# Optimization experiments

Hardware: AMD Instinct MI355X
Metric: run time of the kernel (lower is better)

## Reference

```python
import jax, jax.numpy as jnp
import numpy as np

FS = 512.0
T = 2048
CYC_PHA, CYC_AMP = 3, 6
NBINS = 18
PHA_BANDS = [(2.0 + 2.0 * k, 4.0 + 2.0 * k) for k in range(10)]
AMP_BANDS = [(30.0 + 12.0 * k, 42.0 + 12.0 * k) for k in range(10)]


def _design_filter(fs, low, high, cycle):
    # windowed-sinc bandpass, taps = cycle * fs / low (tensorpac cycle rule), forced odd
    n = int(cycle * fs / low)
    if n % 2 == 0:
        n += 1
    t = np.arange(n) - (n - 1) / 2.0
    lp = lambda fc: 2.0 * fc / fs * np.sinc(2.0 * fc / fs * t)
    h = (lp(high) - lp(low)) * np.hamming(n)
    fc = 0.5 * (low + high)
    h = h / np.abs(np.sum(h * np.exp(-2j * np.pi * fc / fs * t)))  # unit gain at band center
    return h.astype(np.float32)


def _build_kernels():
    filts = [_design_filter(FS, l, h, CYC_PHA) for l, h in PHA_BANDS] + \
            [_design_filter(FS, l, h, CYC_AMP) for l, h in AMP_BANDS]
    L = max(f.shape[0] for f in filts)
    padded = []
    for f in filts:
        p = L - f.shape[0]
        pl = p // 2
        padded.append(np.pad(f, (pl, p - pl)))
    return np.stack(padded)  # (F, L), L odd


def _conv_same(sig, kernels):
    # sig: (N, Tp), kernels: (F, L) -> (N, F, Tp); cross-correlation, 'same' padding (L odd)
    L = kernels.shape[1]
    pad = (L - 1) // 2
    return jax.lax.conv_general_dilated(
        sig[:, None, :], kernels[:, None, :], window_strides=(1,),
        padding=((pad, L - 1 - pad),), dimension_numbers=("NCH", "OIH", "NCH"))


def _analytic(x):
    # FFT-based Hilbert analytic signal along last axis
    n = x.shape[-1]
    h = np.zeros(n, np.float32)
    h[0] = 1.0
    if n % 2 == 0:
        h[n // 2] = 1.0
        h[1:n // 2] = 2.0
    else:
        h[1:(n + 1) // 2] = 2.0
    return jnp.fft.ifft(jnp.fft.fft(x, axis=-1) * h, axis=-1)


def _modulation_index(pha, amp):
    # Tort MI: pha (B,C,P,S,T), amp (B,C,A,S,T) -> (B,C,P,A)
    idx = jnp.clip(jnp.floor((pha + jnp.pi) / (2.0 * jnp.pi) * NBINS), 0, NBINS - 1).astype(jnp.int32)
    sums, cnts = [], []
    for b in range(NBINS):  # fixed small bin count
        m = (idx == b).astype(amp.dtype)                       # (B,C,P,S,T)
        sums.append(jnp.einsum('bcpst,bcast->bcpas', m, amp))  # (B,C,P,A,S)
        cnts.append(m.sum(-1))                                 # (B,C,P,S)
    amp_sum = jnp.stack(sums, -1)                              # (B,C,P,A,S,N)
    cnt = jnp.stack(cnts, -1)[:, :, :, None, :, :]             # (B,C,P,1,S,N)
    amp_mean = amp_sum / jnp.maximum(cnt, 1.0)
    p = amp_mean / jnp.maximum(amp_mean.sum(-1, keepdims=True), 1e-12)
    log_n = jnp.log(jnp.asarray(NBINS, amp.dtype))
    mi = (log_n + (p * jnp.log(jnp.maximum(p, 1e-12))).sum(-1)) / log_n
    return mi.mean(-1)  # average over segments


def setup_inputs() -> dict:
    key = jax.random.key(0)
    x = jax.random.normal(key, (4, 8, 4, T), dtype=jnp.float32)
    kernels = jnp.asarray(_build_kernels())
    return {"x": x, "kernels": kernels}


def reference(x, kernels):
    B, C, S, Tlen = x.shape
    npha = len(PHA_BANDS)
    pad = kernels.shape[1] - 1  # max_padlen (edge_mode)
    sig = x.reshape(B * C * S, Tlen)
    sig = jnp.pad(sig, ((0, 0), (pad, pad)), mode='reflect')
    # filtfilt_mode: average forward conv and time-reversed conv
    fwd = _conv_same(sig, kernels)
    bwd = _conv_same(sig[:, ::-1], kernels)[:, :, ::-1]
    filt = 0.5 * (fwd + bwd)
    filt = filt[:, :, pad:-pad]  # strip edge padding -> (N, F, T)
    ana = _analytic(filt)
    pha = jnp.arctan2(ana.imag[:, :npha], ana.real[:, :npha])
    amp = jnp.sqrt(ana.real[:, npha:] ** 2 + ana.imag[:, npha:] ** 2)
    pha = pha.reshape(B, C, npha, S, Tlen)
    amp = amp.reshape(B, C, len(AMP_BANDS), S, Tlen)
    return _modulation_index(pha, amp)
```

## Files before the change

kernel.cpp:

```cpp
#include <hip/hip_runtime.h>
#include <math.h>

#define TT 2048
#define LK 769
#define NF 20
#define NS 128
#define NB 18

typedef __attribute__((ext_vector_type(8))) short short8;
typedef __attribute__((ext_vector_type(4))) float f32x4;

__device__ __forceinline__ float2 cmul(float2 a, float2 b) {
  return make_float2(a.x * b.x - a.y * b.y, a.x * b.y + a.y * b.x);
}
__device__ __forceinline__ float2 cmulc(float2 a, float2 b) {
  return make_float2(a.x * b.x + a.y * b.y, a.y * b.x - a.x * b.y);
}
#define CADD(a, b) make_float2((a).x + (b).x, (a).y + (b).y)
#define CSUB(a, b) make_float2((a).x - (b).x, (a).y - (b).y)

__global__ __launch_bounds__(256) void prep_kernel(const float* __restrict__ ker,
                                                   float2* __restrict__ tw,
                                                   float* __restrict__ hsym,
                                                   int* __restrict__ rng,
                                                   float* __restrict__ out) {
  __shared__ int red[4][2];
  const int blk = blockIdx.x;
  const int tid = threadIdx.x;
  if (blk < 8) {
    int i = blk * 256 + tid;
    if (i == 0) { tw[0] = make_float2(1.f, 0.f); }
    else {
      int half = 1 << (31 - __clz(i));
      int j = i - half;
      float ang = -3.14159265358979323846f * (float)j / (float)half;
      float s, c;
      sincosf(ang, &s, &c);
      tw[i] = make_float2(c, s);
    }
    int oi = blk * 256 + tid;
    if (oi < 3200) out[oi] = 0.f;
    return;
  }
  if (blk >= 8 && blk < 13) {
    int oi = blk * 256 + tid;
    if (oi < 3200) out[oi] = 0.f;
  }
  if (blk < 13 && blk >= 8) {  }
  const int o = blk - 8;
  if (o >= NF) return;
  const float* kr = ker + o * LK;
  int k0 = 784, k1 = 0;
  for (int k = tid; k < 784; k += 256) {
    float v = 0.f;
    if (k < LK) v = 0.5f * (kr[k] + kr[LK - 1 - k]);
    hsym[o * 784 + k] = v;
    if (v != 0.f) { k0 = min(k0, k); k1 = max(k1, k + 1); }
  }
#pragma unroll
  for (int off = 32; off > 0; off >>= 1) {
    k0 = min(k0, __shfl_down(k0, off));
    k1 = max(k1, __shfl_down(k1, off));
  }
  if ((tid & 63) == 0) { red[tid >> 6][0] = k0; red[tid >> 6][1] = k1; }
  __syncthreads();
  if (tid == 0) {
    k0 = min(min(red[0][0], red[1][0]), min(red[2][0], red[3][0]));
    k1 = max(max(red[0][1], red[1][1]), max(red[2][1], red[3][1]));
    rng[2 * o] = k0 & ~7;
    rng[2 * o + 1] = (k1 + 7) & ~7;
  }
}

__global__ __launch_bounds__(256) void convhil_kernel(const float* __restrict__ x,
                                                      const float* __restrict__ hsym,
                                                      const int* __restrict__ rng,
                                                      const float2* __restrict__ tw,
                                                      float* __restrict__ filt) {
  __shared__ __align__(16) float smem[4096];
  float* w   = smem;
  float2* z  = (float2*)smem;
  const int tid = threadIdx.x;
  const int wv = tid >> 6;
  const int lane = tid & 63;
  const int ord = blockIdx.x;
  const int p = ord / NS;
  const int n = ord % NS;
  const int o1 = p;
  const int o2 = 10 + (9 - p);
  const float* xr = x + n * TT;
  for (int j = tid; j < 2832; j += 256) {
    float v = 0.f;
    if (j < 2816) {
      int m = j - 384;
      if (m < 0) m = -m;
      if (m > 2047) m = 4094 - m;
      v = xr[m];
    }
    w[j] = v;
  }
  const float* h1g = hsym + o1 * 784;
  const float* h2g = hsym + o2 * 784;
  const int A0 = rng[2 * o1], A1 = rng[2 * o1 + 1];
  const int B0 = rng[2 * o2], B1 = rng[2 * o2 + 1];
  const int U0 = min(A0, B0);
  const int U1 = max(A1, B1);
  __syncthreads();

  const int bA = 4 * tid;
  const int bB = 1024 + 4 * tid;
  float acc1A[4], acc1B[4], acc2A[4], acc2B[4];
#pragma unroll
  for (int r = 0; r < 4; ++r) { acc1A[r] = 0.f; acc1B[r] = 0.f; acc2A[r] = 0.f; acc2B[r] = 0.f; }
  if (U0 < U1) {
    float4 a0 = *(const float4*)&w[bA + U0];
    float4 a1 = *(const float4*)&w[bA + U0 + 4];
    float4 a2 = *(const float4*)&w[bA + U0 + 8];
    float4 b0 = *(const float4*)&w[bB + U0];
    float4 b1 = *(const float4*)&w[bB + U0 + 4];
    float4 b2 = *(const float4*)&w[bB + U0 + 8];
    float4 h1a = *(const float4*)&h1g[U0];
    float4 h1b = *(const float4*)&h1g[U0 + 4];
    float4 h2a = *(const float4*)&h2g[U0];
    float4 h2b = *(const float4*)&h2g[U0 + 4];
    for (int k = U0; k < U1; k += 8) {
      float4 a3 = *(const float4*)&w[bA + k + 12];
      float4 a4 = *(const float4*)&w[bA + k + 16];
      float4 b3 = *(const float4*)&w[bB + k + 12];
      float4 b4 = *(const float4*)&w[bB + k + 16];
      float4 h1an = *(const float4*)&h1g[k + 8];
      float4 h1bn = *(const float4*)&h1g[k + 12];
      float4 h2an = *(const float4*)&h2g[k + 8];
      float4 h2bn = *(const float4*)&h2g[k + 12];
      float wa[11] = {a0.x, a0.y, a0.z, a0.w, a1.x, a1.y, a1.z, a1.w,
                      a2.x, a2.y, a2.z};
      float wb[11] = {b0.x, b0.y, b0.z, b0.w, b1.x, b1.y, b1.z, b1.w,
                      b2.x, b2.y, b2.z};
      float h1[8] = {h1a.x, h1a.y, h1a.z, h1a.w, h1b.x, h1b.y, h1b.z, h1b.w};
      float h2[8] = {h2a.x, h2a.y, h2a.z, h2a.w, h2b.x, h2b.y, h2b.z, h2b.w};
      if (k >= A0 && k < A1) {
#pragma unroll
        for (int r = 0; r < 4; ++r) {
#pragma unroll
          for (int j = 0; j < 8; ++j) {
            acc1A[r] = fmaf(h1[j], wa[r + j], acc1A[r]);
            acc1B[r] = fmaf(h1[j], wb[r + j], acc1B[r]);
          }
        }
      }
      if (k >= B0 && k < B1) {
#pragma unroll
        for (int r = 0; r < 4; ++r) {
#pragma unroll
          for (int j = 0; j < 8; ++j) {
            acc2A[r] = fmaf(h2[j], wa[r + j], acc2A[r]);
            acc2B[r] = fmaf(h2[j], wb[r + j], acc2B[r]);
          }
        }
      }
      a0 = a2; a1 = a3; a2 = a4;
      b0 = b2; b1 = b3; b2 = b4;
      h1a = h1an; h1b = h1bn;
      h2a = h2an; h2b = h2bn;
    }
  }
  __syncthreads();
#pragma unroll
  for (int r = 0; r < 4; ++r) {
    z[bA + r] = make_float2(acc1A[r], acc2A[r]);
    z[bB + r] = make_float2(acc1B[r], acc2B[r]);
  }
  __syncthreads();
  const float C = 0.70710678118654752f;
  {
    const int Q = 256;
    const int j = tid & (Q - 1);
    const int base = ((tid & ~(Q - 1)) << 3) + j;
    const float2 x0 = z[base],         x1 = z[base + Q];
    const float2 x2 = z[base + 2 * Q], x3 = z[base + 3 * Q];
    const float2 x4 = z[base + 4 * Q], x5 = z[base + 5 * Q];
    const float2 x6 = z[base + 6 * Q], x7 = z[base + 7 * Q];
    const float2 W1 = tw[4 * Q + j], W2 = tw[2 * Q + j], W4 = tw[Q + j];
    const float2 W3 = cmul(W1, W2);
    const float2 W5 = cmul(W1, W4);
    const float2 W6 = cmul(W2, W4);
    const float2 W7 = cmul(W3, W4);
    const float2 s0 = CADD(x0, x4), s1 = CSUB(x0, x4);
    const float2 s2 = CADD(x2, x6), s3 = CSUB(x2, x6);
    const float2 E0 = CADD(s0, s2), E2 = CSUB(s0, s2);
    const float2 E1 = make_float2(s1.x + s3.y, s1.y - s3.x);
    const float2 E3 = make_float2(s1.x - s3.y, s1.y + s3.x);
    const float2 t0 = CADD(x1, x5), t1 = CSUB(x1, x5);
    const float2 t2 = CADD(x3, x7), t3 = CSUB(x3, x7);
    const float2 O0 = CADD(t0, t2), O2 = CSUB(t0, t2);
    const float2 O1 = make_float2(t1.x + t3.y, t1.y - t3.x);
    const float2 O3 = make_float2(t1.x - t3.y, t1.y + t3.x);
    const float2 wO1 = make_float2(C * (O1.x + O1.y), C * (O1.y - O1.x));
    const float2 w3O3 = make_float2(C * (O3.y - O3.x), -C * (O3.x + O3.y));
    const float2 mO2 = make_float2(O2.y, -O2.x);
    const float2 y0 = CADD(E0, O0), y4 = CSUB(E0, O0);
    const float2 y1 = CADD(E1, wO1), y5 = CSUB(E1, wO1);
    const float2 y2 = CADD(E2, mO2), y6 = CSUB(E2, mO2);
    const float2 y3 = CADD(E3, w3O3), y7 = CSUB(E3, w3O3);
    z[base]         = y0;
    z[base + Q]     = cmul(y1, W1);
    z[base + 2 * Q] = cmul(y2, W2);
    z[base + 3 * Q] = cmul(y3, W3);
    z[base + 4 * Q] = cmul(y4, W4);
    z[base + 5 * Q] = cmul(y5, W5);
    z[base + 6 * Q] = cmul(y6, W6);
    z[base + 7 * Q] = cmul(y7, W7);
  }
  __syncthreads();
#pragma unroll
  for (int st = 0; st < 2; ++st) {
    const int Q = (st == 0) ? 32 : 4;
    const int j = tid & (Q - 1);
    const int base = ((tid & ~(Q - 1)) << 3) + j;
    const float2 x0 = z[base],         x1 = z[base + Q];
    const float2 x2 = z[base + 2 * Q], x3 = z[base + 3 * Q];
    const float2 x4 = z[base + 4 * Q], x5 = z[base + 5 * Q];
    const float2 x6 = z[base + 6 * Q], x7 = z[base + 7 * Q];
    const float2 W1 = tw[4 * Q + j], W2 = tw[2 * Q + j], W4 = tw[Q + j];
    const float2 W3 = cmul(W1, W2);
    const float2 W5 = cmul(W1, W4);
    const float2 W6 = cmul(W2, W4);
    const float2 W7 = cmul(W3, W4);
    const float2 s0 = CADD(x0, x4), s1 = CSUB(x0, x4);
    const float2 s2 = CADD(x2, x6), s3 = CSUB(x2, x6);
    const float2 E0 = CADD(s0, s2), E2 = CSUB(s0, s2);
    const float2 E1 = make_float2(s1.x + s3.y, s1.y - s3.x);
    const float2 E3 = make_float2(s1.x - s3.y, s1.y + s3.x);
    const float2 t0 = CADD(x1, x5), t1 = CSUB(x1, x5);
    const float2 t2 = CADD(x3, x7), t3 = CSUB(x3, x7);
    const float2 O0 = CADD(t0, t2), O2 = CSUB(t0, t2);
    const float2 O1 = make_float2(t1.x + t3.y, t1.y - t3.x);
    const float2 O3 = make_float2(t1.x - t3.y, t1.y + t3.x);
    const float2 wO1 = make_float2(C * (O1.x + O1.y), C * (O1.y - O1.x));
    const float2 w3O3 = make_float2(C * (O3.y - O3.x), -C * (O3.x + O3.y));
    const float2 mO2 = make_float2(O2.y, -O2.x);
    const float2 y0 = CADD(E0, O0), y4 = CSUB(E0, O0);
    const float2 y1 = CADD(E1, wO1), y5 = CSUB(E1, wO1);
    const float2 y2 = CADD(E2, mO2), y6 = CSUB(E2, mO2);
    const float2 y3 = CADD(E3, w3O3), y7 = CSUB(E3, w3O3);
    z[base]         = y0;
    z[base + Q]     = cmul(y1, W1);
    z[base + 2 * Q] = cmul(y2, W2);
    z[base + 3 * Q] = cmul(y3, W3);
    z[base + 4 * Q] = cmul(y4, W4);
    z[base + 5 * Q] = cmul(y5, W5);
    z[base + 6 * Q] = cmul(y6, W6);
    z[base + 7 * Q] = cmul(y7, W7);
    __builtin_amdgcn_wave_barrier();
  }
#pragma unroll
  for (int h = 0; h < 2; ++h) {
    const int bf = 128 * wv + lane + 64 * h;
    const int base = bf << 2;
    const float2 x0 = z[base], x1 = z[base + 1];
    const float2 x2 = z[base + 2], x3 = z[base + 3];
    const float2 t0 = CADD(x0, x2), t1 = CSUB(x0, x2);
    const float2 t2 = CADD(x1, x3), t3 = CSUB(x1, x3);
    z[base]     = CADD(t0, t2);
    z[base + 1] = make_float2(t1.x + t3.y, t1.y - t3.x);
    z[base + 2] = CSUB(t0, t2);
    z[base + 3] = make_float2(t1.x - t3.y, t1.y + t3.x);
  }
  __builtin_amdgcn_wave_barrier();
#pragma unroll
  for (int i = 0; i < 8; ++i) {
    const int pp = 512 * wv + lane + 64 * i;
    if (pp != 0 && pp != 2) {
      if (pp & 2) { z[pp] = make_float2(0.f, 0.f); }
      else        { float2 v = z[pp]; z[pp] = make_float2(2.f * v.x, 2.f * v.y); }
    }
  }
  __builtin_amdgcn_wave_barrier();
#pragma unroll
  for (int h = 0; h < 2; ++h) {
    const int bf = 128 * wv + lane + 64 * h;
    const int base = bf << 2;
    const float2 u0 = z[base], u1 = z[base + 1];
    const float2 u2 = z[base + 2], u3 = z[base + 3];
    const float2 t0 = CADD(u0, u2), t1 = CSUB(u0, u2);
    const float2 t2 = CADD(u1, u3), t3 = CSUB(u1, u3);
    z[base]     = CADD(t0, t2);
    z[base + 1] = make_float2(t1.x - t3.y, t1.y + t3.x);
    z[base + 2] = CSUB(t0, t2);
    z[base + 3] = make_float2(t1.x + t3.y, t1.y - t3.x);
  }
  __builtin_amdgcn_wave_barrier();
#pragma unroll
  for (int st = 0; st < 2; ++st) {
    const int Q = (st == 0) ? 4 : 32;
    const int j = tid & (Q - 1);
    const int base = ((tid & ~(Q - 1)) << 3) + j;
    const float2 W1 = tw[4 * Q + j], W2 = tw[2 * Q + j], W4 = tw[Q + j];
    const float2 W3 = cmul(W1, W2);
    const float2 W5 = cmul(W1, W4);
    const float2 W6 = cmul(W2, W4);
    const float2 W7 = cmul(W3, W4);
    const float2 u0 = z[base];
    const float2 u1 = cmulc(z[base + Q], W1);
    const float2 u2 = cmulc(z[base + 2 * Q], W2);
    const float2 u3 = cmulc(z[base + 3 * Q], W3);
    const float2 u4 = cmulc(z[base + 4 * Q], W4);
    const float2 u5 = cmulc(z[base + 5 * Q], W5);
    const float2 u6 = cmulc(z[base + 6 * Q], W6);
    const float2 u7 = cmulc(z[base + 7 * Q], W7);
    const float2 s0 = CADD(u0, u4), s1 = CSUB(u0, u4);
    const float2 s2 = CADD(u2, u6), s3 = CSUB(u2, u6);
    const float2 E0 = CADD(s0, s2), E2 = CSUB(s0, s2);
    const float2 E1 = make_float2(s1.x - s3.y, s1.y + s3.x);
    const float2 E3 = make_float2(s1.x + s3.y, s1.y - s3.x);
    const float2 t0 = CADD(u1, u5), t1 = CSUB(u1, u5);
    const float2 t2 = CADD(u3, u7), t3 = CSUB(u3, u7);
    const float2 O0 = CADD(t0, t2), O2 = CSUB(t0, t2);
    const float2 O1 = make_float2(t1.x - t3.y, t1.y + t3.x);
    const float2 O3 = make_float2(t1.x + t3.y, t1.y - t3.x);
    const float2 nO1 = make_float2(C * (O1.x - O1.y), C * (O1.x + O1.y));
    const float2 n3O3 = make_float2(-C * (O3.x + O3.y), C * (O3.x - O3.y));
    const float2 iO2 = make_float2(-O2.y, O2.x);
    z[base]         = CADD(E0, O0);
    z[base + 4 * Q] = CSUB(E0, O0);
    z[base + Q]     = CADD(E1, nO1);
    z[base + 5 * Q] = CSUB(E1, nO1);
    z[base + 2 * Q] = CADD(E2, iO2);
    z[base + 6 * Q] = CSUB(E2, iO2);
    z[base + 3 * Q] = CADD(E3, n3O3);
    z[base + 7 * Q] = CSUB(E3, n3O3);
    __builtin_amdgcn_wave_barrier();
  }
  __syncthreads();
  {
    const int Q = 256;
    const int j = tid & (Q - 1);
    const int base = ((tid & ~(Q - 1)) << 3) + j;
    const float2 W1 = tw[4 * Q + j], W2 = tw[2 * Q + j], W4 = tw[Q + j];
    const float2 W3 = cmul(W1, W2);
    const float2 W5 = cmul(W1, W4);
    const float2 W6 = cmul(W2, W4);
    const float2 W7 = cmul(W3, W4);
    const float2 u0 = z[base];
    const float2 u1 = cmulc(z[base + Q], W1);
    const float2 u2 = cmulc(z[base + 2 * Q], W2);
    const float2 u3 = cmulc(z[base + 3 * Q], W3);
    const float2 u4 = cmulc(z[base + 4 * Q], W4);
    const float2 u5 = cmulc(z[base + 5 * Q], W5);
    const float2 u6 = cmulc(z[base + 6 * Q], W6);
    const float2 u7 = cmulc(z[base + 7 * Q], W7);
    const float2 s0 = CADD(u0, u4), s1 = CSUB(u0, u4);
    const float2 s2 = CADD(u2, u6), s3 = CSUB(u2, u6);
    const float2 E0 = CADD(s0, s2), E2 = CSUB(s0, s2);
    const float2 E1 = make_float2(s1.x - s3.y, s1.y + s3.x);
    const float2 E3 = make_float2(s1.x + s3.y, s1.y - s3.x);
    const float2 t0 = CADD(u1, u5), t1 = CSUB(u1, u5);
    const float2 t2 = CADD(u3, u7), t3 = CSUB(u3, u7);
    const float2 O0 = CADD(t0, t2), O2 = CSUB(t0, t2);
    const float2 O1 = make_float2(t1.x - t3.y, t1.y + t3.x);
    const float2 O3 = make_float2(t1.x + t3.y, t1.y - t3.x);
    const float2 nO1 = make_float2(C * (O1.x - O1.y), C * (O1.x + O1.y));
    const float2 n3O3 = make_float2(-C * (O3.x + O3.y), C * (O3.x - O3.y));
    const float2 iO2 = make_float2(-O2.y, O2.x);
    z[base]         = CADD(E0, O0);
    z[base + 4 * Q] = CSUB(E0, O0);
    z[base + Q]     = CADD(E1, nO1);
    z[base + 5 * Q] = CSUB(E1, nO1);
    z[base + 2 * Q] = CADD(E2, iO2);
    z[base + 6 * Q] = CSUB(E2, iO2);
    z[base + 3 * Q] = CADD(E3, n3O3);
    z[base + 7 * Q] = CSUB(E3, n3O3);
  }
  __syncthreads();
  float* out1 = filt + ((size_t)n * NF + o1) * TT;
  float* out2 = filt + ((size_t)n * NF + o2) * TT;
  const float invN = 1.0f / 2048.0f;
  float phA[4], phB[4], amA[4], amB[4];
#pragma unroll
  for (int r = 0; r < 4; ++r) {
    float2 wvA = z[bA + r];
    float h1 = wvA.y * invN - acc2A[r];
    float h2 = acc1A[r] - wvA.x * invN;
    phA[r] = atan2f(h1, acc1A[r]);
    amA[r] = sqrtf(fmaf(acc2A[r], acc2A[r], h2 * h2));
    float2 wvB = z[bB + r];
    float g1 = wvB.y * invN - acc2B[r];
    float g2 = acc1B[r] - wvB.x * invN;
    phB[r] = atan2f(g1, acc1B[r]);
    amB[r] = sqrtf(fmaf(acc2B[r], acc2B[r], g2 * g2));
  }
  *(float4*)&out1[bA] = make_float4(phA[0], phA[1], phA[2], phA[3]);
  *(float4*)&out1[bB] = make_float4(phB[0], phB[1], phB[2], phB[3]);
  *(float4*)&out2[bA] = make_float4(amA[0], amA[1], amA[2], amA[3]);
  *(float4*)&out2[bB] = make_float4(amB[0], amB[1], amB[2], amB[3]);
}

__global__ __launch_bounds__(256) void mi_kernel(const float* __restrict__ filt,
                                                 float* __restrict__ out) {
  __shared__ __align__(16) unsigned int idx32[512];
  __shared__ float Cp[4][12][19];
  const int tid = threadIdx.x;
  const int wave = tid >> 6;
  const int lane = tid & 63;
  const int blk = blockIdx.x;
  const int bc = blk / 40, jp = blk % 40;
  const float* ph = filt + ((size_t)(bc * 4 + jp / 10) * NF + (jp % 10)) * TT;
  for (int g = tid; g < 512; g += 256) {
    float4 v = *(const float4*)&ph[4 * g];
    float vv[4] = {v.x, v.y, v.z, v.w};
    unsigned int packed = 0;
#pragma unroll
    for (int j = 0; j < 4; ++j) {
      int b = (int)floorf((vv[j] + 3.14159274f) / 6.2831855f * 18.0f);
      b = b < 0 ? 0 : (b > 17 ? 17 : b);
      packed |= ((unsigned int)b) << (8 * j);
    }
    idx32[g] = packed;
  }
  __syncthreads();
  const int n16 = lane & 15;
  const int quad = lane >> 4;
  const int aband = n16 < 10 ? n16 : 9;
  const int ja = (jp & 3) + 4 * aband;
  const float* aptr = filt + ((size_t)(bc * 4 + ja / 10) * NF + 10 + (ja % 10)) * TT
                      + quad * 8;
  const bool isAmp = (n16 < 10);
  const bool isOne = (n16 == 10);
  f32x4 acc0 = {0.f, 0.f, 0.f, 0.f};
  f32x4 acc1 = {0.f, 0.f, 0.f, 0.f};
  const int s0 = wave * 16, s1 = s0 + 16;
  float4 p0 = *(const float4*)(aptr + s0 * 32);
  float4 p1 = *(const float4*)(aptr + s0 * 32 + 4);
  for (int s = s0; s < s1; ++s) {
    float4 c0 = p0, c1 = p1;
    if (s < s1 - 1) {
      p0 = *(const float4*)(aptr + (s + 1) * 32);
      p1 = *(const float4*)(aptr + (s + 1) * 32 + 4);
    }
    float a[8] = {c0.x, c0.y, c0.z, c0.w, c1.x, c1.y, c1.z, c1.w};
    short8 ah, am_, al;
#pragma unroll
    for (int j = 0; j < 8; ++j) {
      float v = isAmp ? a[j] : (isOne ? 1.0f : 0.0f);
      unsigned int u = __float_as_uint(v);
      float h = __uint_as_float(u & 0xFFFF0000u);
      float r1 = v - h;
      unsigned int u2 = __float_as_uint(r1);
      float md = __uint_as_float(u2 & 0xFFFF0000u);
      float r2 = r1 - md;
      unsigned int u3 = __float_as_uint(r2);
      ah[j] = (short)(u >> 16);
      am_[j] = (short)(u2 >> 16);
      al[j] = (short)(u3 >> 16);
    }
    const int dw = s * 8 + quad * 2;
    unsigned int d0 = idx32[dw], d1 = idx32[dw + 1];
    short8 b0, b1;
#pragma unroll
    for (int j = 0; j < 8; ++j) {
      unsigned int byte = ((j < 4 ? d0 : d1) >> ((j & 3) * 8)) & 0xFFu;
      b0[j] = (byte == (unsigned int)n16) ? (short)0x3F80 : (short)0;
      b1[j] = (byte == (unsigned int)(n16 + 16)) ? (short)0x3F80 : (short)0;
    }
    acc0 = __builtin_amdgcn_mfma_f32_16x16x32_bf16(ah, b0, acc0, 0, 0, 0);
    acc0 = __builtin_amdgcn_mfma_f32_16x16x32_bf16(am_, b0, acc0, 0, 0, 0);
    acc0 = __builtin_amdgcn_mfma_f32_16x16x32_bf16(al, b0, acc0, 0, 0, 0);
    acc1 = __builtin_amdgcn_mfma_f32_16x16x32_bf16(ah, b1, acc1, 0, 0, 0);
    acc1 = __builtin_amdgcn_mfma_f32_16x16x32_bf16(am_, b1, acc1, 0, 0, 0);
    acc1 = __builtin_amdgcn_mfma_f32_16x16x32_bf16(al, b1, acc1, 0, 0, 0);
  }
#pragma unroll
  for (int r = 0; r < 4; ++r) {
    int row = quad * 4 + r;
    if (row < 11) {
      Cp[wave][row][n16] = acc0[r];
      if (n16 < 2) Cp[wave][row][16 + n16] = acc1[r];
    }
  }
  __syncthreads();
  if (tid < 10) {
    float tot = 0.f, mb_[18];
#pragma unroll
    for (int b = 0; b < 18; ++b) {
      float s = Cp[0][tid][b] + Cp[1][tid][b] + Cp[2][tid][b] + Cp[3][tid][b];
      float c = Cp[0][10][b] + Cp[1][10][b] + Cp[2][10][b] + Cp[3][10][b];
      float mb = s / fmaxf(c, 1.0f);
      mb_[b] = mb; tot += mb;
    }
    tot = fmaxf(tot, 1e-12f);
    float s = 0.f;
#pragma unroll
    for (int b = 0; b < 18; ++b) {
      float pb = mb_[b] / tot;
      s += pb * logf(fmaxf(pb, 1e-12f));
    }
    const float LOGN = 2.8903717578961645f;
    atomicAdd(&out[bc * 100 + (jp >> 2) * 10 + tid],
              0.25f * (LOGN + s) / LOGN);
  }
}

extern "C" void kernel_launch(void* const* d_in, const int* in_sizes, int n_in,
                              void* d_out, int out_size, void* d_ws, size_t ws_size,
                              hipStream_t stream) {
  (void)in_sizes; (void)n_in; (void)out_size; (void)ws_size;
  const float* x = (const float*)d_in[0];
  const float* ker = (const float*)d_in[1];
  float* out = (float*)d_out;
  float* filt = (float*)d_ws;
  float2* tw = (float2*)(filt + (size_t)NS * NF * TT);
  float* hsym = (float*)(tw + TT);
  int* rng = (int*)(hsym + NF * 784);

  prep_kernel<<<28, 256, 0, stream>>>(ker, tw, hsym, rng, out);
  convhil_kernel<<<NS * 10, 256, 0, stream>>>(x, hsym, rng, tw, filt);
  mi_kernel<<<32 * 40, 256, 0, stream>>>(filt, out);
}
```

Baseline: 127.9 us.

## Replace direct FIR convolution with 4096-point FFT convolution

The direct time-domain FIR loop is replaced by FFT-based convolution. A new kernel takes 4096-point FFTs of each symmetrised filter (conjugated and scaled) and of each reflect-padded signal. The conv kernel then multiplies the signal spectrum by a packed pair of filter spectra and runs one inverse FFT to get both filtered outputs as real and imaginary parts. This removes roughly O(L) FMAs per sample, at the cost of an extra kernel launch, larger workspace spectra held in global memory, and a 4096-point inverse FFT per block.

New measurement: 125.9 us. No clear change (-1.5%).

```diff
diff --git a/kernel.cpp b/kernel.cpp
--- a/kernel.cpp
+++ b/kernel.cpp
@@ -6,6 +6,7 @@
 #define NF 20
 #define NS 128
 #define NB 18
+#define NFFT 4096
 
 typedef __attribute__((ext_vector_type(8))) short short8;
 typedef __attribute__((ext_vector_type(4))) float f32x4;
@@ -19,67 +20,173 @@
 #define CADD(a, b) make_float2((a).x + (b).x, (a).y + (b).y)
 #define CSUB(a, b) make_float2((a).x - (b).x, (a).y - (b).y)
 
-__global__ __launch_bounds__(256) void prep_kernel(const float* __restrict__ ker,
-                                                   float2* __restrict__ tw,
-                                                   float* __restrict__ hsym,
-                                                   int* __restrict__ rng,
+__device__ __forceinline__ void fwd_r8(float2* z, const float2* __restrict__ tw,
+                                       int tt, int Q) {
+  const float C = 0.70710678118654752f;
+  const int j = tt & (Q - 1);
+  const int base = ((tt & ~(Q - 1)) << 3) + j;
+  const float2 x0 = z[base],         x1 = z[base + Q];
+  const float2 x2 = z[base + 2 * Q], x3 = z[base + 3 * Q];
+  const float2 x4 = z[base + 4 * Q], x5 = z[base + 5 * Q];
+  const float2 x6 = z[base + 6 * Q], x7 = z[base + 7 * Q];
+  const float2 W1 = tw[4 * Q + j], W2 = tw[2 * Q + j], W4 = tw[Q + j];
+  const float2 W3 = cmul(W1, W2);
+  const float2 W5 = cmul(W1, W4);
+  const float2 W6 = cmul(W2, W4);
+  const float2 W7 = cmul(W3, W4);
+  const float2 s0 = CADD(x0, x4), s1 = CSUB(x0, x4);
+  const float2 s2 = CADD(x2, x6), s3 = CSUB(x2, x6);
+  const float2 E0 = CADD(s0, s2), E2 = CSUB(s0, s2);
+  const float2 E1 = make_float2(s1.x + s3.y, s1.y - s3.x);
+  const float2 E3 = make_float2(s1.x - s3.y, s1.y + s3.x);
+  const float2 t0 = CADD(x1, x5), t1 = CSUB(x1, x5);
+  const float2 t2 = CADD(x3, x7), t3 = CSUB(x3, x7);
+  const float2 O0 = CADD(t0, t2), O2 = CSUB(t0, t2);
+  const float2 O1 = make_float2(t1.x + t3.y, t1.y - t3.x);
+  const float2 O3 = make_float2(t1.x - t3.y, t1.y + t3.x);
+  const float2 wO1 = make_float2(C * (O1.x + O1.y), C * (O1.y - O1.x));
+  const float2 w3O3 = make_float2(C * (O3.y - O3.x), -C * (O3.x + O3.y));
+  const float2 mO2 = make_float2(O2.y, -O2.x);
+  const float2 y0 = CADD(E0, O0), y4 = CSUB(E0, O0);
+  const float2 y1 = CADD(E1, wO1), y5 = CSUB(E1, wO1);
+  const float2 y2 = CADD(E2, mO2), y6 = CSUB(E2, mO2);
+  const float2 y3 = CADD(E3, w3O3), y7 = CSUB(E3, w3O3);
+  z[base]         = y0;
+  z[base + Q]     = cmul(y1, W1);
+  z[base + 2 * Q] = cmul(y2, W2);
+  z[base + 3 * Q] = cmul(y3, W3);
+  z[base + 4 * Q] = cmul(y4, W4);
+  z[base + 5 * Q] = cmul(y5, W5);
+  z[base + 6 * Q] = cmul(y6, W6);
+  z[base + 7 * Q] = cmul(y7, W7);
+}
+
+__device__ __forceinline__ void inv_r8(float2* z, const float2* __restrict__ tw,
+                                       int tt, int Q) {
+  const float C = 0.70710678118654752f;
+  const int j = tt & (Q - 1);
+  const int base = ((tt & ~(Q - 1)) << 3) + j;
+  const float2 W1 = tw[4 * Q + j], W2 = tw[2 * Q + j], W4 = tw[Q + j];
+  const float2 W3 = cmul(W1, W2);
+  const float2 W5 = cmul(W1, W4);
+  const float2 W6 = cmul(W2, W4);
+  const float2 W7 = cmul(W3, W4);
+  const float2 u0 = z[base];
+  const float2 u1 = cmulc(z[base + Q], W1);
+  const float2 u2 = cmulc(z[base + 2 * Q], W2);
+  const float2 u3 = cmulc(z[base + 3 * Q], W3);
+  const float2 u4 = cmulc(z[base + 4 * Q], W4);
+  const float2 u5 = cmulc(z[base + 5 * Q], W5);
+  const float2 u6 = cmulc(z[base + 6 * Q], W6);
+  const float2 u7 = cmulc(z[base + 7 * Q], W7);
+  const float2 s0 = CADD(u0, u4), s1 = CSUB(u0, u4);
+  const float2 s2 = CADD(u2, u6), s3 = CSUB(u2, u6);
+  const float2 E0 = CADD(s0, s2), E2 = CSUB(s0, s2);
+  const float2 E1 = make_float2(s1.x - s3.y, s1.y + s3.x);
+  const float2 E3 = make_float2(s1.x + s3.y, s1.y - s3.x);
+  const float2 t0 = CADD(u1, u5), t1 = CSUB(u1, u5);
+  const float2 t2 = CADD(u3, u7), t3 = CSUB(u3, u7);
+  const float2 O0 = CADD(t0, t2), O2 = CSUB(t0, t2);
+  const float2 O1 = make_float2(t1.x - t3.y, t1.y + t3.x);
+  const float2 O3 = make_float2(t1.x + t3.y, t1.y - t3.x);
+  const float2 nO1 = make_float2(C * (O1.x - O1.y), C * (O1.x + O1.y));
+  const float2 n3O3 = make_float2(-C * (O3.x + O3.y), C * (O3.x - O3.y));
+  const float2 iO2 = make_float2(-O2.y, O2.x);
+  z[base]         = CADD(E0, O0);
+  z[base + 4 * Q] = CSUB(E0, O0);
+  z[base + Q]     = CADD(E1, nO1);
+  z[base + 5 * Q] = CSUB(E1, nO1);
+  z[base + 2 * Q] = CADD(E2, iO2);
+  z[base + 6 * Q] = CSUB(E2, iO2);
+  z[base + 3 * Q] = CADD(E3, n3O3);
+  z[base + 7 * Q] = CSUB(E3, n3O3);
+}
+
+__global__ __launch_bounds__(256) void prep_kernel(float2* __restrict__ tw,
                                                    float* __restrict__ out) {
-  __shared__ int red[4][2];
+  const int i = blockIdx.x * 256 + threadIdx.x;
+  if (i == 0) {
+    tw[0] = make_float2(1.f, 0.f);
+  } else {
+    int half = 1 << (31 - __clz(i));
+    int j = i - half;
+    float ang = -3.14159265358979323846f * (float)j / (float)half;
+    float s, c;
+    sincosf(ang, &s, &c);
+    tw[i] = make_float2(c, s);
+  }
+  if (i < 3200) out[i] = 0.f;
+}
+
+__global__ __launch_bounds__(256) void specf_kernel(const float* __restrict__ x,
+                                                    const float* __restrict__ ker,
+                                                    const float2* __restrict__ tw,
+                                                    float2* __restrict__ Hc,
+                                                    float2* __restrict__ Xs) {
+  __shared__ __align__(16) float2 z[NFFT];
+  const int tid = threadIdx.x;
   const int blk = blockIdx.x;
-  const int tid = threadIdx.x;
-  if (blk < 8) {
-    int i = blk * 256 + tid;
-    if (i == 0) { tw[0] = make_float2(1.f, 0.f); }
-    else {
-      int half = 1 << (31 - __clz(i));
-      int j = i - half;
-      float ang = -3.14159265358979323846f * (float)j / (float)half;
-      float s, c;
-      sincosf(ang, &s, &c);
-      tw[i] = make_float2(c, s);
-    }
-    int oi = blk * 256 + tid;
-    if (oi < 3200) out[oi] = 0.f;
-    return;
-  }
-  if (blk >= 8 && blk < 13) {
-    int oi = blk * 256 + tid;
-    if (oi < 3200) out[oi] = 0.f;
-  }
-  if (blk < 13 && blk >= 8) {  }
-  const int o = blk - 8;
-  if (o >= NF) return;
-  const float* kr = ker + o * LK;
-  int k0 = 784, k1 = 0;
-  for (int k = tid; k < 784; k += 256) {
-    float v = 0.f;
-    if (k < LK) v = 0.5f * (kr[k] + kr[LK - 1 - k]);
-    hsym[o * 784 + k] = v;
-    if (v != 0.f) { k0 = min(k0, k); k1 = max(k1, k + 1); }
-  }
-#pragma unroll
-  for (int off = 32; off > 0; off >>= 1) {
-    k0 = min(k0, __shfl_down(k0, off));
-    k1 = max(k1, __shfl_down(k1, off));
-  }
-  if ((tid & 63) == 0) { red[tid >> 6][0] = k0; red[tid >> 6][1] = k1; }
-  __syncthreads();
-  if (tid == 0) {
-    k0 = min(min(red[0][0], red[1][0]), min(red[2][0], red[3][0]));
-    k1 = max(max(red[0][1], red[1][1]), max(red[2][1], red[3][1]));
-    rng[2 * o] = k0 & ~7;
-    rng[2 * o + 1] = (k1 + 7) & ~7;
-  }
-}
-
-__global__ __launch_bounds__(256) void convhil_kernel(const float* __restrict__ x,
-                                                      const float* __restrict__ hsym,
-                                                      const int* __restrict__ rng,
+  if (blk < NF) {
+    const float* kr = ker + blk * LK;
+#pragma unroll
+    for (int h = 0; h < 16; ++h) {
+      int i = tid + 256 * h;
+      float v = 0.f;
+      if (i < LK) v = 0.5f * (kr[i] + kr[LK - 1 - i]);
+      z[i] = make_float2(v, 0.f);
+    }
+  } else {
+    const float* xr = x + (size_t)(blk - NF) * TT;
+#pragma unroll
+    for (int h = 0; h < 16; ++h) {
+      int i = tid + 256 * h;
+      float v = 0.f;
+      if (i < 2816) {
+        int m = i - 384;
+        if (m < 0) m = -m;
+        if (m > 2047) m = 4094 - m;
+        v = xr[m];
+      }
+      z[i] = make_float2(v, 0.f);
+    }
+  }
+  __syncthreads();
+  fwd_r8(z, tw, tid, 512);
+  fwd_r8(z, tw, tid + 256, 512);
+  __syncthreads();
+  fwd_r8(z, tw, tid, 64);
+  fwd_r8(z, tw, tid + 256, 64);
+  __builtin_amdgcn_wave_barrier();
+  fwd_r8(z, tw, tid, 8);
+  fwd_r8(z, tw, tid + 256, 8);
+  __builtin_amdgcn_wave_barrier();
+  fwd_r8(z, tw, tid, 1);
+  fwd_r8(z, tw, tid + 256, 1);
+  __syncthreads();
+  if (blk < NF) {
+    const float s = 1.0f / 4096.0f;
+    float2* o = Hc + (size_t)blk * NFFT;
+#pragma unroll
+    for (int h = 0; h < 16; ++h) {
+      int i = tid + 256 * h;
+      float2 v = z[i];
+      o[i] = make_float2(v.x * s, -v.y * s);
+    }
+  } else {
+    float2* o = Xs + (size_t)(blk - NF) * NFFT;
+#pragma unroll
+    for (int h = 0; h < 16; ++h) {
+      int i = tid + 256 * h;
+      o[i] = z[i];
+    }
+  }
+}
+
+__global__ __launch_bounds__(256) void convhil_kernel(const float2* __restrict__ Xs,
+                                                      const float2* __restrict__ Hc,
                                                       const float2* __restrict__ tw,
                                                       float* __restrict__ filt) {
-  __shared__ __align__(16) float smem[4096];
-  float* w   = smem;
-  float2* z  = (float2*)smem;
+  __shared__ __align__(16) float2 z[NFFT];
   const int tid = threadIdx.x;
   const int wv = tid >> 6;
   const int lane = tid & 63;
@@ -88,171 +195,47 @@
   const int n = ord % NS;
   const int o1 = p;
   const int o2 = 10 + (9 - p);
-  const float* xr = x + n * TT;
-  for (int j = tid; j < 2832; j += 256) {
-    float v = 0.f;
-    if (j < 2816) {
-      int m = j - 384;
-      if (m < 0) m = -m;
-      if (m > 2047) m = 4094 - m;
-      v = xr[m];
-    }
-    w[j] = v;
-  }
-  const float* h1g = hsym + o1 * 784;
-  const float* h2g = hsym + o2 * 784;
-  const int A0 = rng[2 * o1], A1 = rng[2 * o1 + 1];
-  const int B0 = rng[2 * o2], B1 = rng[2 * o2 + 1];
-  const int U0 = min(A0, B0);
-  const int U1 = max(A1, B1);
-  __syncthreads();
-
+  const float2* Xn = Xs + (size_t)n * NFFT;
+  const float2* H1 = Hc + (size_t)o1 * NFFT;
+  const float2* H2 = Hc + (size_t)o2 * NFFT;
+#pragma unroll
+  for (int h = 0; h < 16; ++h) {
+    int i = tid + 256 * h;
+    float2 Xv = Xn[i];
+    float2 a = H1[i];
+    float2 b = H2[i];
+    float2 Cc = make_float2(a.x - b.y, a.y + b.x);
+    z[i] = cmul(Xv, Cc);
+  }
+  __syncthreads();
+  inv_r8(z, tw, tid, 1);
+  inv_r8(z, tw, tid + 256, 1);
+  __builtin_amdgcn_wave_barrier();
+  inv_r8(z, tw, tid, 8);
+  inv_r8(z, tw, tid + 256, 8);
+  __builtin_amdgcn_wave_barrier();
+  inv_r8(z, tw, tid, 64);
+  inv_r8(z, tw, tid + 256, 64);
+  __syncthreads();
+  inv_r8(z, tw, tid, 512);
+  inv_r8(z, tw, tid + 256, 512);
+  __syncthreads();
   const int bA = 4 * tid;
   const int bB = 1024 + 4 * tid;
   float acc1A[4], acc1B[4], acc2A[4], acc2B[4];
 #pragma unroll
-  for (int r = 0; r < 4; ++r) { acc1A[r] = 0.f; acc1B[r] = 0.f; acc2A[r] = 0.f; acc2B[r] = 0.f; }
-  if (U0 < U1) {
-    float4 a0 = *(const float4*)&w[bA + U0];
-    float4 a1 = *(const float4*)&w[bA + U0 + 4];
-    float4 a2 = *(const float4*)&w[bA + U0 + 8];
-    float4 b0 = *(const float4*)&w[bB + U0];
-    float4 b1 = *(const float4*)&w[bB + U0 + 4];
-    float4 b2 = *(const float4*)&w[bB + U0 + 8];
-    float4 h1a = *(const float4*)&h1g[U0];
-    float4 h1b = *(const float4*)&h1g[U0 + 4];
-    float4 h2a = *(const float4*)&h2g[U0];
-    float4 h2b = *(const float4*)&h2g[U0 + 4];
-    for (int k = U0; k < U1; k += 8) {
-      float4 a3 = *(const float4*)&w[bA + k + 12];
-      float4 a4 = *(const float4*)&w[bA + k + 16];
-      float4 b3 = *(const float4*)&w[bB + k + 12];
-      float4 b4 = *(const float4*)&w[bB + k + 16];
-      float4 h1an = *(const float4*)&h1g[k + 8];
-      float4 h1bn = *(const float4*)&h1g[k + 12];
-      float4 h2an = *(const float4*)&h2g[k + 8];
-      float4 h2bn = *(const float4*)&h2g[k + 12];
-      float wa[11] = {a0.x, a0.y, a0.z, a0.w, a1.x, a1.y, a1.z, a1.w,
-                      a2.x, a2.y, a2.z};
-      float wb[11] = {b0.x, b0.y, b0.z, b0.w, b1.x, b1.y, b1.z, b1.w,
-                      b2.x, b2.y, b2.z};
-      float h1[8] = {h1a.x, h1a.y, h1a.z, h1a.w, h1b.x, h1b.y, h1b.z, h1b.w};
-      float h2[8] = {h2a.x, h2a.y, h2a.z, h2a.w, h2b.x, h2b.y, h2b.z, h2b.w};
-      if (k >= A0 && k < A1) {
-#pragma unroll
-        for (int r = 0; r < 4; ++r) {
-#pragma unroll
-          for (int j = 0; j < 8; ++j) {
-            acc1A[r] = fmaf(h1[j], wa[r + j], acc1A[r]);
-            acc1B[r] = fmaf(h1[j], wb[r + j], acc1B[r]);
-          }
-        }
-      }
-      if (k >= B0 && k < B1) {
-#pragma unroll
-        for (int r = 0; r < 4; ++r) {
-#pragma unroll
-          for (int j = 0; j < 8; ++j) {
-            acc2A[r] = fmaf(h2[j], wa[r + j], acc2A[r]);
-            acc2B[r] = fmaf(h2[j], wb[r + j], acc2B[r]);
-          }
-        }
-      }
-      a0 = a2; a1 = a3; a2 = a4;
-      b0 = b2; b1 = b3; b2 = b4;
-      h1a = h1an; h1b = h1bn;
-      h2a = h2an; h2b = h2bn;
-    }
-  }
-  __syncthreads();
-#pragma unroll
   for (int r = 0; r < 4; ++r) {
-    z[bA + r] = make_float2(acc1A[r], acc2A[r]);
-    z[bB + r] = make_float2(acc1B[r], acc2B[r]);
+    float2 vA = z[bA + r]; acc1A[r] = vA.x; acc2A[r] = vA.y;
+    float2 vB = z[bB + r]; acc1B[r] = vB.x; acc2B[r] = vB.y;
   }
   __syncthreads();
   const float C = 0.70710678118654752f;
-  {
-    const int Q = 256;
-    const int j = tid & (Q - 1);
-    const int base = ((tid & ~(Q - 1)) << 3) + j;
-    const float2 x0 = z[base],         x1 = z[base + Q];
-    const float2 x2 = z[base + 2 * Q], x3 = z[base + 3 * Q];
-    const float2 x4 = z[base + 4 * Q], x5 = z[base + 5 * Q];
-    const float2 x6 = z[base + 6 * Q], x7 = z[base + 7 * Q];
-    const float2 W1 = tw[4 * Q + j], W2 = tw[2 * Q + j], W4 = tw[Q + j];
-    const float2 W3 = cmul(W1, W2);
-    const float2 W5 = cmul(W1, W4);
-    const float2 W6 = cmul(W2, W4);
-    const float2 W7 = cmul(W3, W4);
-    const float2 s0 = CADD(x0, x4), s1 = CSUB(x0, x4);
-    const float2 s2 = CADD(x2, x6), s3 = CSUB(x2, x6);
-    const float2 E0 = CADD(s0, s2), E2 = CSUB(s0, s2);
-    const float2 E1 = make_float2(s1.x + s3.y, s1.y - s3.x);
-    const float2 E3 = make_float2(s1.x - s3.y, s1.y + s3.x);
-    const float2 t0 = CADD(x1, x5), t1 = CSUB(x1, x5);
-    const float2 t2 = CADD(x3, x7), t3 = CSUB(x3, x7);
-    const float2 O0 = CADD(t0, t2), O2 = CSUB(t0, t2);
-    const float2 O1 = make_float2(t1.x + t3.y, t1.y - t3.x);
-    const float2 O3 = make_float2(t1.x - t3.y, t1.y + t3.x);
-    const float2 wO1 = make_float2(C * (O1.x + O1.y), C * (O1.y - O1.x));
-    const float2 w3O3 = make_float2(C * (O3.y - O3.x), -C * (O3.x + O3.y));
-    const float2 mO2 = make_float2(O2.y, -O2.x);
-    const float2 y0 = CADD(E0, O0), y4 = CSUB(E0, O0);
-    const float2 y1 = CADD(E1, wO1), y5 = CSUB(E1, wO1);
-    const float2 y2 = CADD(E2, mO2), y6 = CSUB(E2, mO2);
-    const float2 y3 = CADD(E3, w3O3), y7 = CSUB(E3, w3O3);
-    z[base]         = y0;
-    z[base + Q]     = cmul(y1, W1);
-    z[base + 2 * Q] = cmul(y2, W2);
-    z[base + 3 * Q] = cmul(y3, W3);
-    z[base + 4 * Q] = cmul(y4, W4);
-    z[base + 5 * Q] = cmul(y5, W5);
-    z[base + 6 * Q] = cmul(y6, W6);
-    z[base + 7 * Q] = cmul(y7, W7);
-  }
-  __syncthreads();
-#pragma unroll
-  for (int st = 0; st < 2; ++st) {
-    const int Q = (st == 0) ? 32 : 4;
-    const int j = tid & (Q - 1);
-    const int base = ((tid & ~(Q - 1)) << 3) + j;
-    const float2 x0 = z[base],         x1 = z[base + Q];
-    const float2 x2 = z[base + 2 * Q], x3 = z[base + 3 * Q];
-    const float2 x4 = z[base + 4 * Q], x5 = z[base + 5 * Q];
-    const float2 x6 = z[base + 6 * Q], x7 = z[base + 7 * Q];
-    const float2 W1 = tw[4 * Q + j], W2 = tw[2 * Q + j], W4 = tw[Q + j];
-    const float2 W3 = cmul(W1, W2);
-    const float2 W5 = cmul(W1, W4);
-    const float2 W6 = cmul(W2, W4);
-    const float2 W7 = cmul(W3, W4);
-    const float2 s0 = CADD(x0, x4), s1 = CSUB(x0, x4);
-    const float2 s2 = CADD(x2, x6), s3 = CSUB(x2, x6);
-    const float2 E0 = CADD(s0, s2), E2 = CSUB(s0, s2);
-    const float2 E1 = make_float2(s1.x + s3.y, s1.y - s3.x);
-    const float2 E3 = make_float2(s1.x - s3.y, s1.y + s3.x);
-    const float2 t0 = CADD(x1, x5), t1 = CSUB(x1, x5);
-    const float2 t2 = CADD(x3, x7), t3 = CSUB(x3, x7);
-    const float2 O0 = CADD(t0, t2), O2 = CSUB(t0, t2);
-    const float2 O1 = make_float2(t1.x + t3.y, t1.y - t3.x);
-    const float2 O3 = make_float2(t1.x - t3.y, t1.y + t3.x);
-    const float2 wO1 = make_float2(C * (O1.x + O1.y), C * (O1.y - O1.x));
-    const float2 w3O3 = make_float2(C * (O3.y - O3.x), -C * (O3.x + O3.y));
-    const float2 mO2 = make_float2(O2.y, -O2.x);
-    const float2 y0 = CADD(E0, O0), y4 = CSUB(E0, O0);
-    const float2 y1 = CADD(E1, wO1), y5 = CSUB(E1, wO1);
-    const float2 y2 = CADD(E2, mO2), y6 = CSUB(E2, mO2);
-    const float2 y3 = CADD(E3, w3O3), y7 = CSUB(E3, w3O3);
-    z[base]         = y0;
-    z[base + Q]     = cmul(y1, W1);
-    z[base + 2 * Q] = cmul(y2, W2);
-    z[base + 3 * Q] = cmul(y3, W3);
-    z[base + 4 * Q] = cmul(y4, W4);
-    z[base + 5 * Q] = cmul(y5, W5);
-    z[base + 6 * Q] = cmul(y6, W6);
-    z[base + 7 * Q] = cmul(y7, W7);
-    __builtin_amdgcn_wave_barrier();
-  }
+  fwd_r8(z, tw, tid, 256);
+  __syncthreads();
+  fwd_r8(z, tw, tid, 32);
+  __builtin_amdgcn_wave_barrier();
+  fwd_r8(z, tw, tid, 4);
+  __builtin_amdgcn_wave_barrier();
 #pragma unroll
   for (int h = 0; h < 2; ++h) {
     const int bf = 128 * wv + lane + 64 * h;
@@ -290,88 +273,14 @@
     z[base + 3] = make_float2(t1.x + t3.y, t1.y - t3.x);
   }
   __builtin_amdgcn_wave_barrier();
-#pragma unroll
-  for (int st = 0; st < 2; ++st) {
-    const int Q = (st == 0) ? 4 : 32;
-    const int j = tid & (Q - 1);
-    const int base = ((tid & ~(Q - 1)) << 3) + j;
-    const float2 W1 = tw[4 * Q + j], W2 = tw[2 * Q + j], W4 = tw[Q + j];
-    const float2 W3 = cmul(W1, W2);
-    const float2 W5 = cmul(W1, W4);
-    const float2 W6 = cmul(W2, W4);
-    const float2 W7 = cmul(W3, W4);
-    const float2 u0 = z[base];
-    const float2 u1 = cmulc(z[base + Q], W1);
-    const float2 u2 = cmulc(z[base + 2 * Q], W2);
-    const float2 u3 = cmulc(z[base + 3 * Q], W3);
-    const float2 u4 = cmulc(z[base + 4 * Q], W4);
-    const float2 u5 = cmulc(z[base + 5 * Q], W5);
-    const float2 u6 = cmulc(z[base + 6 * Q], W6);
-    const float2 u7 = cmulc(z[base + 7 * Q], W7);
-    const float2 s0 = CADD(u0, u4), s1 = CSUB(u0, u4);
-    const float2 s2 = CADD(u2, u6), s3 = CSUB(u2, u6);
-    const float2 E0 = CADD(s0, s2), E2 = CSUB(s0, s2);
-    const float2 E1 = make_float2(s1.x - s3.y, s1.y + s3.x);
-    const float2 E3 = make_float2(s1.x + s3.y, s1.y - s3.x);
-    const float2 t0 = CADD(u1, u5), t1 = CSUB(u1, u5);
-    const float2 t2 = CADD(u3, u7), t3 = CSUB(u3, u7);
-    const float2 O0 = CADD(t0, t2), O2 = CSUB(t0, t2);
-    const float2 O1 = make_float2(t1.x - t3.y, t1.y + t3.x);
-    const float2 O3 = make_float2(t1.x + t3.y, t1.y - t3.x);
-    const float2 nO1 = make_float2(C * (O1.x - O1.y), C * (O1.x + O1.y));
-    const float2 n3O3 = make_float2(-C * (O3.x + O3.y), C * (O3.x - O3.y));
-    const float2 iO2 = make_float2(-O2.y, O2.x);
-    z[base]         = CADD(E0, O0);
-    z[base + 4 * Q] = CSUB(E0, O0);
-    z[base + Q]     = CADD(E1, nO1);
-    z[base + 5 * Q] = CSUB(E1, nO1);
-    z[base + 2 * Q] = CADD(E2, iO2);
-    z[base + 6 * Q] = CSUB(E2, iO2);
-    z[base + 3 * Q] = CADD(E3, n3O3);
-    z[base + 7 * Q] = CSUB(E3, n3O3);
-    __builtin_amdgcn_wave_barrier();
-  }
-  __syncthreads();
-  {
-    const int Q = 256;
-    const int j = tid & (Q - 1);
-    const int base = ((tid & ~(Q - 1)) << 3) + j;
-    const float2 W1 = tw[4 * Q + j], W2 = tw[2 * Q + j], W4 = tw[Q + j];
-    const float2 W3 = cmul(W1, W2);
-    const float2 W5 = cmul(W1, W4);
-    const float2 W6 = cmul(W2, W4);
-    const float2 W7 = cmul(W3, W4);
-    const float2 u0 = z[base];
-    const float2 u1 = cmulc(z[base + Q], W1);
-    const float2 u2 = cmulc(z[base + 2 * Q], W2);
-    const float2 u3 = cmulc(z[base + 3 * Q], W3);
-    const float2 u4 = cmulc(z[base + 4 * Q], W4);
-    const float2 u5 = cmulc(z[base + 5 * Q], W5);
-    const float2 u6 = cmulc(z[base + 6 * Q], W6);
-    const float2 u7 = cmulc(z[base + 7 * Q], W7);
-    const float2 s0 = CADD(u0, u4), s1 = CSUB(u0, u4);
-    const float2 s2 = CADD(u2, u6), s3 = CSUB(u2, u6);
-    const float2 E0 = CADD(s0, s2), E2 = CSUB(s0, s2);
-    const float2 E1 = make_float2(s1.x - s3.y, s1.y + s3.x);
-    const float2 E3 = make_float2(s1.x + s3.y, s1.y - s3.x);
-    const float2 t0 = CADD(u1, u5), t1 = CSUB(u1, u5);
-    const float2 t2 = CADD(u3, u7), t3 = CSUB(u3, u7);
-    const float2 O0 = CADD(t0, t2), O2 = CSUB(t0, t2);
-    const float2 O1 = make_float2(t1.x - t3.y, t1.y + t3.x);
-    const float2 O3 = make_float2(t1.x + t3.y, t1.y - t3.x);
-    const float2 nO1 = make_float2(C * (O1.x - O1.y), C * (O1.x + O1.y));
-    const float2 n3O3 = make_float2(-C * (O3.x + O3.y), C * (O3.x - O3.y));
-    const float2 iO2 = make_float2(-O2.y, O2.x);
-    z[base]         = CADD(E0, O0);
-    z[base + 4 * Q] = CSUB(E0, O0);
-    z[base + Q]     = CADD(E1, nO1);
-    z[base + 5 * Q] = CSUB(E1, nO1);
-    z[base + 2 * Q] = CADD(E2, iO2);
-    z[base + 6 * Q] = CSUB(E2, iO2);
-    z[base + 3 * Q] = CADD(E3, n3O3);
-    z[base + 7 * Q] = CSUB(E3, n3O3);
-  }
-  __syncthreads();
+  inv_r8(z, tw, tid, 4);
+  __builtin_amdgcn_wave_barrier();
+  inv_r8(z, tw, tid, 32);
+  __builtin_amdgcn_wave_barrier();
+  __syncthreads();
+  inv_r8(z, tw, tid, 256);
+  __syncthreads();
+  (void)C;
   float* out1 = filt + ((size_t)n * NF + o1) * TT;
   float* out2 = filt + ((size_t)n * NF + o2) * TT;
   const float invN = 1.0f / 2048.0f;
@@ -509,10 +418,11 @@
   float* out = (float*)d_out;
   float* filt = (float*)d_ws;
   float2* tw = (float2*)(filt + (size_t)NS * NF * TT);
-  float* hsym = (float*)(tw + TT);
-  int* rng = (int*)(hsym + NF * 784);
-
-  prep_kernel<<<28, 256, 0, stream>>>(ker, tw, hsym, rng, out);
-  convhil_kernel<<<NS * 10, 256, 0, stream>>>(x, hsym, rng, tw, filt);
+  float2* Hc = tw + NFFT;
+  float2* Xs = Hc + (size_t)NF * NFFT;
+
+  prep_kernel<<<16, 256, 0, stream>>>(tw, out);
+  specf_kernel<<<NF + NS, 256, 0, stream>>>(x, ker, tw, Hc, Xs);
+  convhil_kernel<<<NS * 10, 256, 0, stream>>>(Xs, Hc, tw, filt);
   mi_kernel<<<32 * 40, 256, 0, stream>>>(filt, out);
 }
```
